# Optimization experiments

Hardware: AMD Instinct MI355X
Metric: run time of the kernel (lower is better)

## Reference

```python
import jax, jax.numpy as jnp
import numpy as np

EPS = 1e-5
KS = 3  # deformable kernel size
K2 = KS * KS


def conv2d(x, w, stride=1, padding=1):
    return jax.lax.conv_general_dilated(
        x, w, window_strides=(stride, stride),
        padding=[(padding, padding), (padding, padding)],
        dimension_numbers=("NCHW", "OIHW", "NCHW"))


def batchnorm(x, gamma, beta):
    # training-mode BN: batch statistics over (N, H, W)
    mean = jnp.mean(x, axis=(0, 2, 3), keepdims=True)
    var = jnp.var(x, axis=(0, 2, 3), keepdims=True)
    xhat = (x - mean) * jax.lax.rsqrt(var + EPS)
    return xhat * gamma[None, :, None, None] + beta[None, :, None, None]


def deform_conv(x, offsets, w, pad=1):
    # x: (B,C,H,W); offsets: (B,2*K2,H,W) -> first K2 channels = row (y)
    # offsets, next K2 = col (x) offsets; w: (O,C,KS,KS)
    B, C, H, W = x.shape
    xp = jnp.pad(x, ((0, 0), (0, 0), (pad, pad), (pad, pad)))
    Hp, Wp = H + 2 * pad, W + 2 * pad
    # base grid (center of each output pixel in padded coords)
    p0_y = jnp.arange(H, dtype=x.dtype) + pad            # (H,)
    p0_x = jnp.arange(W, dtype=x.dtype) + pad            # (W,)
    # kernel tap offsets in [-1, 0, 1]^2, row-major
    pn = jnp.stack(jnp.meshgrid(jnp.arange(KS) - pad, jnp.arange(KS) - pad,
                                indexing="ij"), axis=-1).reshape(K2, 2).astype(x.dtype)
    off = offsets.reshape(B, 2, K2, H, W)
    off_y = jnp.transpose(off[:, 0], (0, 2, 3, 1))       # (B,H,W,K2)
    off_x = jnp.transpose(off[:, 1], (0, 2, 3, 1))
    py = p0_y[None, :, None, None] + pn[:, 0][None, None, None, :] + off_y
    px = p0_x[None, None, :, None] + pn[:, 1][None, None, None, :] + off_x
    py = jnp.clip(py, 0.0, Hp - 1.0)
    px = jnp.clip(px, 0.0, Wp - 1.0)
    y0 = jnp.floor(py).astype(jnp.int32)
    x0 = jnp.floor(px).astype(jnp.int32)
    y1 = jnp.minimum(y0 + 1, Hp - 1)
    x1 = jnp.minimum(x0 + 1, Wp - 1)
    wy = (py - y0.astype(x.dtype))[:, None]              # (B,1,H,W,K2)
    wx = (px - x0.astype(x.dtype))[:, None]

    def gather(xb, yi, xi):                              # xb (C,Hp,Wp)
        return xb[:, yi, xi]                             # (C,H,W,K2)
    g = jax.vmap(gather)
    v00 = g(xp, y0, x0)
    v01 = g(xp, y0, x1)
    v10 = g(xp, y1, x0)
    v11 = g(xp, y1, x1)
    sampled = (v00 * (1 - wy) * (1 - wx) + v01 * (1 - wy) * wx +
               v10 * wy * (1 - wx) + v11 * wy * wx)      # (B,C,H,W,K2)
    return jnp.einsum("bchwk,ock->bohw", sampled, w.reshape(w.shape[0], C, K2))


def setup_inputs() -> dict:
    key = jax.random.key(0)
    ks = jax.random.split(key, 16)
    B, Cin, P, H, W = 64, 64, 64, 64, 64
    s = lambda k, shp, fan: jax.random.normal(k, shp, jnp.float32) * (fan ** -0.5)
    return {
        "x": jax.random.normal(ks[0], (B, Cin, H, W), jnp.float32),
        "conv1_w": s(ks[1], (P, Cin, 3, 3), Cin * 9),
        "bn1_g": jnp.ones((P,), jnp.float32), "bn1_b": jnp.zeros((P,), jnp.float32),
        "conv2_w": s(ks[2], (16, P, 1, 1), P),
        "bn2_g": jnp.ones((16,), jnp.float32), "bn2_b": jnp.zeros((16,), jnp.float32),
        "off_w": s(ks[3], (18, 16, 3, 3), 16 * 9) * 0.1,
        "off_b": jnp.zeros((18,), jnp.float32),
        "conv3_w": s(ks[4], (16, 16, 3, 3), 16 * 9),
        "bn3_g": jnp.ones((16,), jnp.float32), "bn3_b": jnp.zeros((16,), jnp.float32),
        "conv4_w": s(ks[5], (P, 16, 3, 3), 16 * 9),
        "bn4_g": jnp.ones((P,), jnp.float32), "bn4_b": jnp.zeros((P,), jnp.float32),
    }


def reference(x, conv1_w, bn1_g, bn1_b, conv2_w, bn2_g, bn2_b, off_w, off_b,
              conv3_w, bn3_g, bn3_b, conv4_w, bn4_g, bn4_b):
    out = jax.nn.relu(batchnorm(conv2d(x, conv1_w, 1, 1), bn1_g, bn1_b))
    out = jax.nn.relu(batchnorm(conv2d(out, conv2_w, 1, 0), bn2_g, bn2_b))
    offsets = conv2d(out, off_w, 1, 1) + off_b[None, :, None, None]
    out = jax.nn.relu(batchnorm(deform_conv(out, offsets, conv3_w), bn3_g, bn3_b))
    out = batchnorm(conv2d(out, conv4_w, 1, 1), bn4_g, bn4_b)
    out = out + x  # identity shortcut (stride=1, in_planes==planes)
    return jax.nn.relu(out)
```

## Files before the change

kernel.cpp:

```cpp
#include <hip/hip_runtime.h>

#define BN_N 262144.0f

typedef unsigned short u16;
typedef __attribute__((ext_vector_type(8))) short short8;
typedef __attribute__((ext_vector_type(4))) float floatx4;

static __device__ __forceinline__ u16 f2bf(float f) {
  union { float f; unsigned u; } v; v.f = f;
  unsigned u = v.u;
  return (u16)((u + 0x7FFFu + ((u >> 16) & 1u)) >> 16);
}
static __device__ __forceinline__ float bf2f(u16 h) {
  union { unsigned u; float f; } v; v.u = ((unsigned)h) << 16;
  return v.f;
}

__global__ __launch_bounds__(256) void prep_w_k(const float* __restrict__ w1,
                                                u16* __restrict__ Bsw) {
  int d = blockIdx.x * 256 + threadIdx.x;
  int kin = d & 7, n = (d >> 3) & 63, kgrp = (d >> 9) & 3, kc = d >> 11;
  int k = kc * 32 + kgrp * 8 + kin;
  int tap = k >> 6, c = k & 63;
  Bsw[d] = f2bf(w1[n * 576 + c * 9 + tap]);
}

__global__ __launch_bounds__(256) void prep_w4_k(const float* __restrict__ w4,
                                                 u16* __restrict__ Bsw4) {
  int d = blockIdx.x * 256 + threadIdx.x;
  if (d >= 10240) return;
  int kin = d & 7, n = (d >> 3) & 63, lk = (d >> 9) & 3, kk = d >> 11;
  int tap = kk * 2 + (lk >> 1);
  int c = ((lk & 1) << 3) + kin;
  float v = (tap < 9) ? w4[n * 144 + c * 9 + tap] : 0.f;
  Bsw4[d] = f2bf(v);
}

__global__ __launch_bounds__(256) void prep_w3_k(const float* __restrict__ w3,
                                                 u16* __restrict__ Bsw3) {
  int d = blockIdx.x * 256 + threadIdx.x;
  if (d >= 2560) return;
  int kin = d & 7, n = (d >> 3) & 15, lk = (d >> 7) & 3, kk = d >> 9;
  int k = kk * 32 + lk * 8 + kin;
  int tap = k >> 4, c = k & 15;
  float v = (tap < 9) ? w3[n * 144 + c * 9 + tap] : 0.f;
  Bsw3[d] = f2bf(v);
}

__global__ __launch_bounds__(256) void prep_wo_k(const float* __restrict__ ow,
                                                 u16* __restrict__ BswO) {
  int d = blockIdx.x * 256 + threadIdx.x;
  if (d >= 5120) return;
  int kin = d & 7, n = (d >> 3) & 31, lk = (d >> 8) & 3, kk = d >> 10;
  int tap = kk * 2 + (lk >> 1);
  int c = ((lk & 1) << 3) + kin;
  float v = (tap < 9 && n < 18) ? ow[n * 144 + c * 9 + tap] : 0.f;
  BswO[d] = f2bf(v);
}

__global__ __launch_bounds__(256) void prep_x_k(const float* __restrict__ x,
                                                u16* __restrict__ xp) {
  int yp = blockIdx.x;
  int b = blockIdx.y;
  int tid = threadIdx.x;
  u16* rowbase = xp + ((size_t)(b * 66 + yp)) * 66 * 64;
  if (yp == 0 || yp == 65) {
    for (int i = tid; i < 1056; i += 256)
      ((ushort4*)rowbase)[i] = make_ushort4(0, 0, 0, 0);
    return;
  }
  int y = yp - 1;
  __shared__ u16 s[64][68];
  for (int i = tid; i < 4096; i += 256) {
    int c = i >> 6, xx = i & 63;
    s[xx][c] = f2bf(x[((b * 64 + c) << 12) + (y << 6) + xx]);
  }
  if (tid < 128) {
    int c = tid & 63;
    int xpad = (tid >> 6) ? 65 : 0;
    rowbase[xpad * 64 + c] = 0;
  }
  __syncthreads();
  for (int j = tid; j < 1024; j += 256) {
    int xx = j >> 4, c4 = (j & 15) << 2;
    *(ushort4*)(rowbase + (xx + 1) * 64 + c4) =
        make_ushort4(s[xx][c4], s[xx][c4 + 1], s[xx][c4 + 2], s[xx][c4 + 3]);
  }
}

__global__ __launch_bounds__(256) void conv1_mfma(const u16* __restrict__ xp,
                                                  const u16* __restrict__ Bsw,
                                                  u16* __restrict__ h1,
                                                  float* __restrict__ sum1, float* __restrict__ sq1) {
  const int tid = threadIdx.x;
  const int w = tid >> 6, l = tid & 63;
  const int lm = l & 15, lk = l >> 4;
  const int b = blockIdx.x >> 4;
  const int y = ((blockIdx.x & 15) << 2) + w;
  const u16* xpb = xp + (size_t)b * 66 * 66 * 64;

  floatx4 acc[4][4];
#pragma unroll
  for (int mt = 0; mt < 4; ++mt)
#pragma unroll
    for (int nb = 0; nb < 4; ++nb)
      acc[mt][nb] = (floatx4){0.f, 0.f, 0.f, 0.f};

  short8 aC[4], bC[4], aN[4], bN[4];

#define C1_LOAD(KK, A, BV)                                              \
  {                                                                     \
    const int tap_ = (KK) >> 1;                                         \
    const int dy_ = tap_ / 3, dx_ = tap_ - dy_ * 3;                     \
    const int c0_ = (((KK) & 1) << 5) + (lk << 3);                      \
    const u16* rowp_ = xpb + (((y + dy_) * 66) + lm + dx_) * 64 + c0_;  \
    A[0] = *(const short8*)(rowp_);                                     \
    A[1] = *(const short8*)(rowp_ + 16 * 64);                           \
    A[2] = *(const short8*)(rowp_ + 32 * 64);                           \
    A[3] = *(const short8*)(rowp_ + 48 * 64);                           \
    const u16* bp_ = Bsw + ((((KK) * 4 + lk) * 64) + lm) * 8;           \
    BV[0] = *(const short8*)(bp_);                                      \
    BV[1] = *(const short8*)(bp_ + 128);                                \
    BV[2] = *(const short8*)(bp_ + 256);                                \
    BV[3] = *(const short8*)(bp_ + 384);                                \
  }

  C1_LOAD(0, aC, bC)
#pragma unroll
  for (int kk = 0; kk < 18; ++kk) {
    if (kk < 17) C1_LOAD(kk + 1, aN, bN)
#pragma unroll
    for (int mt = 0; mt < 4; ++mt)
#pragma unroll
      for (int nb = 0; nb < 4; ++nb)
        acc[mt][nb] = __builtin_amdgcn_mfma_f32_16x16x32_bf16(aC[mt], bC[nb], acc[mt][nb], 0, 0, 0);
#pragma unroll
    for (int i = 0; i < 4; ++i) { aC[i] = aN[i]; bC[i] = bN[i]; }
  }
#undef C1_LOAD

#pragma unroll
  for (int mt = 0; mt < 4; ++mt)
#pragma unroll
    for (int nb = 0; nb < 4; ++nb) {
      u16* dst = h1 + ((size_t)(b * 64 + nb * 16 + lm) << 12) + (y << 6) + mt * 16 + (lk << 2);
      floatx4 v = acc[mt][nb];
      *(ushort4*)dst = make_ushort4(f2bf(v.x), f2bf(v.y), f2bf(v.z), f2bf(v.w));
    }

  __shared__ float lsum[4][64], lsq[4][64];
  float s[4], s2[4];
#pragma unroll
  for (int nb = 0; nb < 4; ++nb) {
    s[nb] = 0.f; s2[nb] = 0.f;
#pragma unroll
    for (int mt = 0; mt < 4; ++mt) {
      floatx4 a = acc[mt][nb];
      s[nb] += a.x + a.y + a.z + a.w;
      s2[nb] += a.x * a.x + a.y * a.y + a.z * a.z + a.w * a.w;
    }
    s[nb] += __shfl_xor(s[nb], 16, 64);  s[nb] += __shfl_xor(s[nb], 32, 64);
    s2[nb] += __shfl_xor(s2[nb], 16, 64); s2[nb] += __shfl_xor(s2[nb], 32, 64);
  }
  if (lk == 0) {
#pragma unroll
    for (int nb = 0; nb < 4; ++nb) { lsum[w][nb * 16 + lm] = s[nb]; lsq[w][nb * 16 + lm] = s2[nb]; }
  }
  __syncthreads();
  if (tid < 64) atomicAdd(&sum1[tid], lsum[0][tid] + lsum[1][tid] + lsum[2][tid] + lsum[3][tid]);
  else if (tid < 128) { int o = tid - 64; atomicAdd(&sq1[o], lsq[0][o] + lsq[1][o] + lsq[2][o] + lsq[3][o]); }
}

__global__ __launch_bounds__(256) void conv2_k(const u16* __restrict__ h1,
                                               const float* __restrict__ w2,
                                               const float* __restrict__ sum1, const float* __restrict__ sq1,
                                               const float* __restrict__ g1, const float* __restrict__ b1,
                                               float* __restrict__ out,
                                               float* __restrict__ sum2, float* __restrict__ sq2) {
  __shared__ float s_wt[64 * 16];
  __shared__ float s_scale[64], s_shift[64];
  __shared__ float ls[4][16], lsq[4][16];
  int tid = threadIdx.x;
  for (int i = tid; i < 1024; i += 256) {
    int o = i >> 6, c = i & 63;
    s_wt[c * 16 + o] = w2[i];
  }
  if (tid < 64) {
    float m = sum1[tid] / BN_N;
    float var = sq1[tid] / BN_N - m * m;
    float sc = g1[tid] * rsqrtf(var + 1e-5f);
    s_scale[tid] = sc;
    s_shift[tid] = b1[tid] - m * sc;
  }
  __syncthreads();
  int p = blockIdx.x * 256 + tid;
  int b = p >> 12, r = p & 4095;
  const u16* src = h1 + ((size_t)b << 18) + r;
  float acc[16];
#pragma unroll
  for (int o = 0; o < 16; ++o) acc[o] = 0.f;
  for (int c = 0; c < 64; ++c) {
    float v = bf2f(src[c << 12]);
    v = fmaxf(v * s_scale[c] + s_shift[c], 0.f);
    const float* wp = &s_wt[c * 16];
    float4 w0 = *(const float4*)wp;
    float4 w1 = *(const float4*)(wp + 4);
    float4 w2v = *(const float4*)(wp + 8);
    float4 w3v = *(const float4*)(wp + 12);
    acc[0] += w0.x * v;  acc[1] += w0.y * v;  acc[2] += w0.z * v;  acc[3] += w0.w * v;
    acc[4] += w1.x * v;  acc[5] += w1.y * v;  acc[6] += w1.z * v;  acc[7] += w1.w * v;
    acc[8] += w2v.x * v; acc[9] += w2v.y * v; acc[10] += w2v.z * v; acc[11] += w2v.w * v;
    acc[12] += w3v.x * v; acc[13] += w3v.y * v; acc[14] += w3v.z * v; acc[15] += w3v.w * v;
  }
  float* dst = out + (size_t)p * 16;
#pragma unroll
  for (int c4 = 0; c4 < 4; ++c4)
    *(float4*)(dst + c4 * 4) = make_float4(acc[c4*4], acc[c4*4+1], acc[c4*4+2], acc[c4*4+3]);
  int lane = tid & 63, wv = tid >> 6;
#pragma unroll
  for (int o = 0; o < 16; ++o) {
    float s = acc[o], s2 = acc[o] * acc[o];
#pragma unroll
    for (int off = 32; off > 0; off >>= 1) {
      s += __shfl_down(s, off, 64);
      s2 += __shfl_down(s2, off, 64);
    }
    if (lane == 0) { ls[wv][o] = s; lsq[wv][o] = s2; }
  }
  __syncthreads();
  if (tid < 16) atomicAdd(&sum2[tid], ls[0][tid] + ls[1][tid] + ls[2][tid] + ls[3][tid]);
  else if (tid < 32) {
    int o = tid - 16;
    atomicAdd(&sq2[o], lsq[0][o] + lsq[1][o] + lsq[2][o] + lsq[3][o]);
  }
}

__global__ __launch_bounds__(256) void bnrelu2_k(const float* __restrict__ ws2,
                                                 const float* __restrict__ sum2, const float* __restrict__ sq2,
                                                 const float* __restrict__ g2, const float* __restrict__ b2,
                                                 u16* __restrict__ h2p) {
  __shared__ float s_scale[16], s_shift[16];
  int tid = threadIdx.x;
  if (tid < 16) {
    float m = sum2[tid] / BN_N;
    float var = sq2[tid] / BN_N - m * m;
    float sc = g2[tid] * rsqrtf(var + 1e-5f);
    s_scale[tid] = sc;
    s_shift[tid] = b2[tid] - m * sc;
  }
  __syncthreads();
  int p = blockIdx.x * 256 + tid;
  int b = p >> 12, r = p & 4095;
  int y = r >> 6, xx = r & 63;
  const float* src = ws2 + (size_t)p * 16;
  u16* dst = h2p + (size_t)(((b * 66) + y + 1) * 66 + xx + 1) * 16;
#pragma unroll
  for (int c4 = 0; c4 < 4; ++c4) {
    float4 v = *(const float4*)(src + c4 * 4);
    u16 o0 = f2bf(fmaxf(v.x * s_scale[c4*4]   + s_shift[c4*4],   0.f));
    u16 o1 = f2bf(fmaxf(v.y * s_scale[c4*4+1] + s_shift[c4*4+1], 0.f));
    u16 o2 = f2bf(fmaxf(v.z * s_scale[c4*4+2] + s_shift[c4*4+2], 0.f));
    u16 o3 = f2bf(fmaxf(v.w * s_scale[c4*4+3] + s_shift[c4*4+3], 0.f));
    *(ushort4*)(dst + c4 * 4) = make_ushort4(o0, o1, o2, o3);
  }
}

__global__ __launch_bounds__(256) void offconv_mfma(const u16* __restrict__ h2p,
                                                    const u16* __restrict__ BswO,
                                                    const float* __restrict__ ob,
                                                    float* __restrict__ offs) {
  const int tid = threadIdx.x;
  const int w = tid >> 6, l = tid & 63;
  const int lm = l & 15, lk = l >> 4;
  const int b = blockIdx.x >> 4;
  const int y = ((blockIdx.x & 15) << 2) + w;
  const u16* hb = h2p + (size_t)b * 66 * 66 * 16;

  floatx4 acc[4][2];
#pragma unroll
  for (int mt = 0; mt < 4; ++mt)
#pragma unroll
    for (int nb = 0; nb < 2; ++nb)
      acc[mt][nb] = (floatx4){0.f, 0.f, 0.f, 0.f};

  short8 aC[4], bC[2], aN[4], bN[2];

#define OC_LOAD(KK, A, BV)                                                    \
  {                                                                           \
    int tap_ = (KK) * 2 + (lk >> 1);                                          \
    if (tap_ > 8) tap_ = 8;                                                   \
    const int dy_ = tap_ / 3, dx_ = tap_ - dy_ * 3;                           \
    const int c0_ = (lk & 1) << 3;                                            \
    const u16* rowp_ = hb + (size_t)(((y + dy_) * 66) + lm + dx_) * 16 + c0_; \
    A[0] = *(const short8*)(rowp_);                                           \
    A[1] = *(const short8*)(rowp_ + 16 * 16);                                 \
    A[2] = *(const short8*)(rowp_ + 32 * 16);                                 \
    A[3] = *(const short8*)(rowp_ + 48 * 16);                                 \
    const u16* bp_ = BswO + ((((KK) * 4 + lk) * 32) + lm) * 8;                \
    BV[0] = *(const short8*)(bp_);                                            \
    BV[1] = *(const short8*)(bp_ + 128);                                      \
  }

  OC_LOAD(0, aC, bC)
#pragma unroll
  for (int kk = 0; kk < 5; ++kk) {
    if (kk < 4) OC_LOAD(kk + 1, aN, bN)
#pragma unroll
    for (int mt = 0; mt < 4; ++mt)
#pragma unroll
      for (int nb = 0; nb < 2; ++nb)
        acc[mt][nb] = __builtin_amdgcn_mfma_f32_16x16x32_bf16(aC[mt], bC[nb], acc[mt][nb], 0, 0, 0);
#pragma unroll
    for (int i = 0; i < 4; ++i) aC[i] = aN[i];
    bC[0] = bN[0]; bC[1] = bN[1];
  }
#undef OC_LOAD

#pragma unroll
  for (int mt = 0; mt < 4; ++mt)
#pragma unroll
    for (int nb = 0; nb < 2; ++nb) {
      int oc = nb * 16 + lm;
      if (oc < 18) {
        float bias = ob[oc];
        floatx4 v = acc[mt][nb];
        v.x += bias; v.y += bias; v.z += bias; v.w += bias;
        float* dst = offs + (size_t)b * 73728 + (oc << 12) + (y << 6) + mt * 16 + (lk << 2);
        *(floatx4*)dst = v;
      }
    }
}

__global__ __launch_bounds__(256) void deform_mfma(const u16* __restrict__ h2p,
                                                   const float* __restrict__ offs,
                                                   const u16* __restrict__ Bsw3,
                                                   float* __restrict__ out,
                                                   float* __restrict__ sum3, float* __restrict__ sq3) {
  const int tid = threadIdx.x;
  const int w = tid >> 6, l = tid & 63;
  const int lm = l & 15, lk = l >> 4;
  const int pbase = blockIdx.x * 256 + w * 64;
  const int b = pbase >> 12;
  const u16* img = h2p + (size_t)b * 66 * 66 * 16;
  const float* offp = offs + (size_t)b * 73728;

  short8 bf[5];
#pragma unroll
  for (int kk = 0; kk < 5; ++kk)
    bf[kk] = *(const short8*)(Bsw3 + (((kk * 4 + lk) * 16) + lm) * 8);

  floatx4 acc[4];
#pragma unroll
  for (int mt = 0; mt < 4; ++mt) acc[mt] = (floatx4){0.f, 0.f, 0.f, 0.f};

#pragma unroll
  for (int mt = 0; mt < 4; ++mt) {
    const int p = pbase + mt * 16 + lm;
    const int r = p & 4095;
    const int y = r >> 6, x = r & 63;
#pragma unroll
    for (int kk = 0; kk < 5; ++kk) {
      const int k0 = kk * 32 + lk * 8;
      int tap = k0 >> 4;
      const int c0 = k0 & 15;
      if (tap > 8) tap = 8;
      const int dy = tap / 3, dx = tap - dy * 3;
      float offy = offp[(tap << 12) + r];
      float offx = offp[((tap + 9) << 12) + r];
      float py = (float)(y + dy) + offy;
      float px = (float)(x + dx) + offx;
      py = fminf(fmaxf(py, 0.f), 65.f);
      px = fminf(fmaxf(px, 0.f), 65.f);
      float y0f = floorf(py), x0f = floorf(px);
      int y0 = (int)y0f, x0 = (int)x0f;
      int y1 = min(y0 + 1, 65), x1 = min(x0 + 1, 65);
      float wy = py - y0f, wx = px - x0f;
      float w00 = (1.f - wy) * (1.f - wx), w01 = (1.f - wy) * wx;
      float w10 = wy * (1.f - wx),         w11 = wy * wx;
      short8 v00 = *(const short8*)(img + (y0 * 66 + x0) * 16 + c0);
      short8 v01 = *(const short8*)(img + (y0 * 66 + x1) * 16 + c0);
      short8 v10 = *(const short8*)(img + (y1 * 66 + x0) * 16 + c0);
      short8 v11 = *(const short8*)(img + (y1 * 66 + x1) * 16 + c0);
      short8 a;
#pragma unroll
      for (int j = 0; j < 8; ++j) {
        float s = bf2f((u16)v00[j]) * w00 + bf2f((u16)v01[j]) * w01
                + bf2f((u16)v10[j]) * w10 + bf2f((u16)v11[j]) * w11;
        a[j] = (short)f2bf(s);
      }
      acc[mt] = __builtin_amdgcn_mfma_f32_16x16x32_bf16(a, bf[kk], acc[mt], 0, 0, 0);
    }
  }

  float s = 0.f, s2 = 0.f;
#pragma unroll
  for (int mt = 0; mt < 4; ++mt) {
    floatx4 a = acc[mt];
    s += a.x + a.y + a.z + a.w;
    s2 += a.x * a.x + a.y * a.y + a.z * a.z + a.w * a.w;
#pragma unroll
    for (int reg = 0; reg < 4; ++reg) {
      int pp = pbase + mt * 16 + lk * 4 + reg;
      out[(size_t)pp * 16 + lm] = acc[mt][reg];
    }
  }
  __shared__ float ls[4][16], lsq[4][16];
  s += __shfl_xor(s, 16, 64);  s += __shfl_xor(s, 32, 64);
  s2 += __shfl_xor(s2, 16, 64); s2 += __shfl_xor(s2, 32, 64);
  if (lk == 0) { ls[w][lm] = s; lsq[w][lm] = s2; }
  __syncthreads();
  if (tid < 16) atomicAdd(&sum3[tid], ls[0][tid] + ls[1][tid] + ls[2][tid] + ls[3][tid]);
  else if (tid < 32) {
    int o = tid - 16;
    atomicAdd(&sq3[o], lsq[0][o] + lsq[1][o] + lsq[2][o] + lsq[3][o]);
  }
}

__global__ __launch_bounds__(256) void bnrelu3_k(const float* __restrict__ wsd,
                                                 const float* __restrict__ sum3, const float* __restrict__ sq3,
                                                 const float* __restrict__ g3, const float* __restrict__ b3,
                                                 u16* __restrict__ h3p) {
  __shared__ float s_scale[16], s_shift[16];
  int tid = threadIdx.x;
  if (tid < 16) {
    float m = sum3[tid] / BN_N;
    float var = sq3[tid] / BN_N - m * m;
    float sc = g3[tid] * rsqrtf(var + 1e-5f);
    s_scale[tid] = sc;
    s_shift[tid] = b3[tid] - m * sc;
  }
  __syncthreads();
  int p = blockIdx.x * 256 + tid;
  int b = p >> 12, r = p & 4095;
  int y = r >> 6, xx = r & 63;
  const float* src = wsd + (size_t)p * 16;
  u16* dst = h3p + (size_t)(((b * 66) + y + 1) * 66 + xx + 1) * 16;
#pragma unroll
  for (int c4 = 0; c4 < 4; ++c4) {
    float4 v = *(const float4*)(src + c4 * 4);
    u16 o0 = f2bf(fmaxf(v.x * s_scale[c4*4]   + s_shift[c4*4],   0.f));
    u16 o1 = f2bf(fmaxf(v.y * s_scale[c4*4+1] + s_shift[c4*4+1], 0.f));
    u16 o2 = f2bf(fmaxf(v.z * s_scale[c4*4+2] + s_shift[c4*4+2], 0.f));
    u16 o3 = f2bf(fmaxf(v.w * s_scale[c4*4+3] + s_shift[c4*4+3], 0.f));
    *(ushort4*)(dst + c4 * 4) = make_ushort4(o0, o1, o2, o3);
  }
}

__global__ __launch_bounds__(256) void conv4_mfma(const u16* __restrict__ h3p,
                                                  const u16* __restrict__ Bsw4,
                                                  u16* __restrict__ h4,
                                                  float* __restrict__ sum4, float* __restrict__ sq4) {
  const int tid = threadIdx.x;
  const int w = tid >> 6, l = tid & 63;
  const int lm = l & 15, lk = l >> 4;
  const int b = blockIdx.x >> 4;
  const int y = ((blockIdx.x & 15) << 2) + w;
  const u16* hb = h3p + (size_t)b * 66 * 66 * 16;

  floatx4 acc[4][4];
#pragma unroll
  for (int mt = 0; mt < 4; ++mt)
#pragma unroll
    for (int nb = 0; nb < 4; ++nb)
      acc[mt][nb] = (floatx4){0.f, 0.f, 0.f, 0.f};

  short8 aC[4], bC[4], aN[4], bN[4];

#define C4_LOAD(KK, A, BV)                                                    \
  {                                                                           \
    int tap_ = (KK) * 2 + (lk >> 1);                                          \
    if (tap_ > 8) tap_ = 8;                                                   \
    const int dy_ = tap_ / 3, dx_ = tap_ - dy_ * 3;                           \
    const int c0_ = (lk & 1) << 3;                                            \
    const u16* rowp_ = hb + (size_t)(((y + dy_) * 66) + lm + dx_) * 16 + c0_; \
    A[0] = *(const short8*)(rowp_);                                           \
    A[1] = *(const short8*)(rowp_ + 16 * 16);                                 \
    A[2] = *(const short8*)(rowp_ + 32 * 16);                                 \
    A[3] = *(const short8*)(rowp_ + 48 * 16);                                 \
    const u16* bp_ = Bsw4 + ((((KK) * 4 + lk) * 64) + lm) * 8;                \
    BV[0] = *(const short8*)(bp_);                                            \
    BV[1] = *(const short8*)(bp_ + 128);                                      \
    BV[2] = *(const short8*)(bp_ + 256);                                      \
    BV[3] = *(const short8*)(bp_ + 384);                                      \
  }

  C4_LOAD(0, aC, bC)
#pragma unroll
  for (int kk = 0; kk < 5; ++kk) {
    if (kk < 4) C4_LOAD(kk + 1, aN, bN)
#pragma unroll
    for (int mt = 0; mt < 4; ++mt)
#pragma unroll
      for (int nb = 0; nb < 4; ++nb)
        acc[mt][nb] = __builtin_amdgcn_mfma_f32_16x16x32_bf16(aC[mt], bC[nb], acc[mt][nb], 0, 0, 0);
#pragma unroll
    for (int i = 0; i < 4; ++i) { aC[i] = aN[i]; bC[i] = bN[i]; }
  }
#undef C4_LOAD

#pragma unroll
  for (int mt = 0; mt < 4; ++mt)
#pragma unroll
    for (int nb = 0; nb < 4; ++nb) {
      u16* dst = h4 + ((size_t)(b * 64 + nb * 16 + lm) << 12) + (y << 6) + mt * 16 + (lk << 2);
      floatx4 v = acc[mt][nb];
      *(ushort4*)dst = make_ushort4(f2bf(v.x), f2bf(v.y), f2bf(v.z), f2bf(v.w));
    }

  __shared__ float lsum[4][64], lsq[4][64];
  float s[4], s2[4];
#pragma unroll
  for (int nb = 0; nb < 4; ++nb) {
    s[nb] = 0.f; s2[nb] = 0.f;
#pragma unroll
    for (int mt = 0; mt < 4; ++mt) {
      floatx4 a = acc[mt][nb];
      s[nb] += a.x + a.y + a.z + a.w;
      s2[nb] += a.x * a.x + a.y * a.y + a.z * a.z + a.w * a.w;
    }
    s[nb] += __shfl_xor(s[nb], 16, 64);  s[nb] += __shfl_xor(s[nb], 32, 64);
    s2[nb] += __shfl_xor(s2[nb], 16, 64); s2[nb] += __shfl_xor(s2[nb], 32, 64);
  }
  if (lk == 0) {
#pragma unroll
    for (int nb = 0; nb < 4; ++nb) { lsum[w][nb * 16 + lm] = s[nb]; lsq[w][nb * 16 + lm] = s2[nb]; }
  }
  __syncthreads();
  if (tid < 64) atomicAdd(&sum4[tid], lsum[0][tid] + lsum[1][tid] + lsum[2][tid] + lsum[3][tid]);
  else if (tid < 128) { int o = tid - 64; atomicAdd(&sq4[o], lsq[0][o] + lsq[1][o] + lsq[2][o] + lsq[3][o]); }
}

__global__ __launch_bounds__(256) void final_k(const u16* __restrict__ h4,
                                               float* __restrict__ out,
                                               const float* __restrict__ x,
                                               const float* __restrict__ sum4, const float* __restrict__ sq4,
                                               const float* __restrict__ g4, const float* __restrict__ b4) {
  __shared__ float s_scale[64], s_shift[64];
  int tid = threadIdx.x;
  if (tid < 64) {
    float m = sum4[tid] / BN_N;
    float var = sq4[tid] / BN_N - m * m;
    float sc = g4[tid] * rsqrtf(var + 1e-5f);
    s_scale[tid] = sc;
    s_shift[tid] = b4[tid] - m * sc;
  }
  __syncthreads();
  int i = (blockIdx.x * 256 + tid) * 4;
  int c = (i >> 12) & 63;
  ushort4 q = *(const ushort4*)(h4 + i);
  float4 xv = *(const float4*)(x + i);
  float sc = s_scale[c], sh = s_shift[c];
  float4 v;
  v.x = fmaxf(bf2f(q.x) * sc + sh + xv.x, 0.f);
  v.y = fmaxf(bf2f(q.y) * sc + sh + xv.y, 0.f);
  v.z = fmaxf(bf2f(q.z) * sc + sh + xv.z, 0.f);
  v.w = fmaxf(bf2f(q.w) * sc + sh + xv.w, 0.f);
  *(float4*)(out + i) = v;
}

extern "C" void kernel_launch(void* const* d_in, const int* in_sizes, int n_in,
                              void* d_out, int out_size, void* d_ws, size_t ws_size,
                              hipStream_t stream) {
  const float* x  = (const float*)d_in[0];
  const float* w1 = (const float*)d_in[1];
  const float* g1 = (const float*)d_in[2];
  const float* b1 = (const float*)d_in[3];
  const float* w2 = (const float*)d_in[4];
  const float* g2 = (const float*)d_in[5];
  const float* b2 = (const float*)d_in[6];
  const float* ow = (const float*)d_in[7];
  const float* ob = (const float*)d_in[8];
  const float* w3 = (const float*)d_in[9];
  const float* g3 = (const float*)d_in[10];
  const float* b3 = (const float*)d_in[11];
  const float* w4 = (const float*)d_in[12];
  const float* g4 = (const float*)d_in[13];
  const float* b4 = (const float*)d_in[14];
  float* out = (float*)d_out;
  float* ws = (float*)d_ws;

  float* offs = ws;
  float* wsd  = offs + 4718592;
  float* ws2  = wsd + 4194304;
  float* h2pf = ws2 + 4194304;
  float* stats = h2pf + 4460544;
  float* sum1 = stats, *sq1 = stats + 64;
  float* sum2 = stats + 128, *sq2 = stats + 144;
  float* sum3 = stats + 160, *sq3 = stats + 176;
  float* sum4 = stats + 192, *sq4 = stats + 256;
  u16* xp   = (u16*)ws;
  u16* Bsw  = (u16*)(stats + 320);
  u16* Bsw4 = Bsw + 36864;
  u16* Bsw3 = Bsw4 + 10240;
  u16* BswO = Bsw3 + 2560;
  u16* h2p  = (u16*)h2pf;
  u16* h4   = (u16*)offs;
  u16* h1   = (u16*)out;

  hipMemsetAsync(stats, 0, 320 * sizeof(float), stream);
  hipMemsetAsync(h2p, 0, 4460544 * sizeof(u16), stream);

  prep_w_k<<<144, 256, 0, stream>>>(w1, Bsw);
  prep_w4_k<<<40, 256, 0, stream>>>(w4, Bsw4);
  prep_w3_k<<<10, 256, 0, stream>>>(w3, Bsw3);
  prep_wo_k<<<20, 256, 0, stream>>>(ow, BswO);
  prep_x_k<<<dim3(66, 64), 256, 0, stream>>>(x, xp);
  conv1_mfma<<<1024, 256, 0, stream>>>(xp, Bsw, h1, sum1, sq1);
  conv2_k<<<1024, 256, 0, stream>>>(h1, w2, sum1, sq1, g1, b1, ws2, sum2, sq2);
  bnrelu2_k<<<1024, 256, 0, stream>>>(ws2, sum2, sq2, g2, b2, h2p);
  offconv_mfma<<<1024, 256, 0, stream>>>(h2p, BswO, ob, offs);
  deform_mfma<<<1024, 256, 0, stream>>>(h2p, offs, Bsw3, wsd, sum3, sq3);
  bnrelu3_k<<<1024, 256, 0, stream>>>(wsd, sum3, sq3, g3, b3, h2p );
  conv4_mfma<<<1024, 256, 0, stream>>>(h2p, Bsw4, h4, sum4, sq4);
  final_k<<<16384, 256, 0, stream>>>(h4, out, x, sum4, sq4, g4, b4);
}
```

Baseline: 361.5 us.

## Stage conv input rows in LDS via global_load_lds with swizzled/padded layouts

The conv1, offset-conv and conv4 kernels now copy their input row band (and, for the small convs, their weights) into shared memory with direct global-to-LDS loads, then read MFMA operands from LDS instead of issuing repeated global loads per tap. The padded input layouts change to support this: the 64-channel buffer uses an XOR chunk swizzle and the 16-channel buffer pads each pixel to 24 elements to reduce bank conflicts. The deform and bnrelu kernels are updated to the new stride. This adds large LDS allocations that may limit occupancy and drops the software register prefetch of A operands. It also grows the memset of the padded buffer.

```diff
diff --git a/kernel.cpp b/kernel.cpp
--- a/kernel.cpp
+++ b/kernel.cpp
@@ -5,6 +5,12 @@
 typedef unsigned short u16;
 typedef __attribute__((ext_vector_type(8))) short short8;
 typedef __attribute__((ext_vector_type(4))) float floatx4;
+
+#define RP1 4224
+#define IS1 278784
+#define RP2 1584
+#define IS2 104544
+#define H2P_TOTAL 6690816
 
 static __device__ __forceinline__ u16 f2bf(float f) {
   union { float f; unsigned u; } v; v.f = f;
@@ -14,6 +20,10 @@
 static __device__ __forceinline__ float bf2f(u16 h) {
   union { unsigned u; float f; } v; v.u = ((unsigned)h) << 16;
   return v.f;
+}
+static __device__ __forceinline__ void cp16(const u16* g, u16* l) {
+  __builtin_amdgcn_global_load_lds((const __attribute__((address_space(1))) unsigned int*)g,
+                                   (__attribute__((address_space(3))) unsigned int*)l, 16, 0, 0);
 }
 
 __global__ __launch_bounds__(256) void prep_w_k(const float* __restrict__ w1,
@@ -63,28 +73,29 @@
   int yp = blockIdx.x;
   int b = blockIdx.y;
   int tid = threadIdx.x;
-  u16* rowbase = xp + ((size_t)(b * 66 + yp)) * 66 * 64;
+  u16* rowbase = xp + (size_t)(b * 66 + yp) * RP1;
   if (yp == 0 || yp == 65) {
-    for (int i = tid; i < 1056; i += 256)
+    for (int i = tid; i < RP1 / 4; i += 256)
       ((ushort4*)rowbase)[i] = make_ushort4(0, 0, 0, 0);
     return;
   }
   int y = yp - 1;
-  __shared__ u16 s[64][68];
+  __shared__ __align__(16) u16 s[64][72];
   for (int i = tid; i < 4096; i += 256) {
     int c = i >> 6, xx = i & 63;
     s[xx][c] = f2bf(x[((b * 64 + c) << 12) + (y << 6) + xx]);
   }
   if (tid < 128) {
     int c = tid & 63;
-    int xpad = (tid >> 6) ? 65 : 0;
-    rowbase[xpad * 64 + c] = 0;
-  }
-  __syncthreads();
-  for (int j = tid; j < 1024; j += 256) {
-    int xx = j >> 4, c4 = (j & 15) << 2;
-    *(ushort4*)(rowbase + (xx + 1) * 64 + c4) =
-        make_ushort4(s[xx][c4], s[xx][c4 + 1], s[xx][c4 + 2], s[xx][c4 + 3]);
+    int pxp = (tid >> 6) ? 65 : 0;
+    rowbase[pxp * 64 + c] = 0;
+  }
+  __syncthreads();
+  for (int j = tid; j < 512; j += 256) {
+    int xx = j >> 3, chunk = j & 7;
+    int pxp = xx + 1;
+    int ph = chunk ^ (pxp & 7);
+    *(short8*)(rowbase + pxp * 64 + ph * 8) = *(const short8*)(&s[xx][chunk * 8]);
   }
 }
 
@@ -92,12 +103,17 @@
                                                   const u16* __restrict__ Bsw,
                                                   u16* __restrict__ h1,
                                                   float* __restrict__ sum1, float* __restrict__ sq1) {
+  __shared__ __align__(16) u16 lA[25600];
   const int tid = threadIdx.x;
   const int w = tid >> 6, l = tid & 63;
   const int lm = l & 15, lk = l >> 4;
   const int b = blockIdx.x >> 4;
-  const int y = ((blockIdx.x & 15) << 2) + w;
-  const u16* xpb = xp + (size_t)b * 66 * 66 * 64;
+  const int y0 = (blockIdx.x & 15) << 2;
+  const int y = y0 + w;
+  const u16* src = xp + ((size_t)b * 66 + y0) * RP1;
+  for (int seg = w; seg < 50; seg += 4)
+    cp16(src + seg * 512 + l * 8, lA + seg * 512);
+  __syncthreads();
 
   floatx4 acc[4][4];
 #pragma unroll
@@ -106,38 +122,39 @@
     for (int nb = 0; nb < 4; ++nb)
       acc[mt][nb] = (floatx4){0.f, 0.f, 0.f, 0.f};
 
-  short8 aC[4], bC[4], aN[4], bN[4];
-
-#define C1_LOAD(KK, A, BV)                                              \
-  {                                                                     \
-    const int tap_ = (KK) >> 1;                                         \
-    const int dy_ = tap_ / 3, dx_ = tap_ - dy_ * 3;                     \
-    const int c0_ = (((KK) & 1) << 5) + (lk << 3);                      \
-    const u16* rowp_ = xpb + (((y + dy_) * 66) + lm + dx_) * 64 + c0_;  \
-    A[0] = *(const short8*)(rowp_);                                     \
-    A[1] = *(const short8*)(rowp_ + 16 * 64);                           \
-    A[2] = *(const short8*)(rowp_ + 32 * 64);                           \
-    A[3] = *(const short8*)(rowp_ + 48 * 64);                           \
-    const u16* bp_ = Bsw + ((((KK) * 4 + lk) * 64) + lm) * 8;           \
-    BV[0] = *(const short8*)(bp_);                                      \
-    BV[1] = *(const short8*)(bp_ + 128);                                \
-    BV[2] = *(const short8*)(bp_ + 256);                                \
-    BV[3] = *(const short8*)(bp_ + 384);                                \
-  }
-
-  C1_LOAD(0, aC, bC)
+  short8 bC[4], bN[4];
+#define BLOAD(KK, BV)                                                 \
+  { const u16* bp_ = Bsw + ((((KK) * 4 + lk) * 64) + lm) * 8;         \
+    BV[0] = *(const short8*)(bp_);                                    \
+    BV[1] = *(const short8*)(bp_ + 128);                              \
+    BV[2] = *(const short8*)(bp_ + 256);                              \
+    BV[3] = *(const short8*)(bp_ + 384); }
+
+  BLOAD(0, bC)
 #pragma unroll
   for (int kk = 0; kk < 18; ++kk) {
-    if (kk < 17) C1_LOAD(kk + 1, aN, bN)
+    if (kk < 17) BLOAD(kk + 1, bN)
+    const int tap = kk >> 1;
+    const int dy = (tap < 3) ? 0 : ((tap < 6) ? 1 : 2);
+    const int dx = tap - dy * 3;
+    const int chunk = ((kk & 1) << 2) + lk;
+    const int rowoff = (w + dy) * RP1;
+    short8 aF[4];
+#pragma unroll
+    for (int mt = 0; mt < 4; ++mt) {
+      int pxp = mt * 16 + lm + dx;
+      int ph = chunk ^ (pxp & 7);
+      aF[mt] = *(const short8*)(lA + rowoff + pxp * 64 + ph * 8);
+    }
 #pragma unroll
     for (int mt = 0; mt < 4; ++mt)
 #pragma unroll
       for (int nb = 0; nb < 4; ++nb)
-        acc[mt][nb] = __builtin_amdgcn_mfma_f32_16x16x32_bf16(aC[mt], bC[nb], acc[mt][nb], 0, 0, 0);
-#pragma unroll
-    for (int i = 0; i < 4; ++i) { aC[i] = aN[i]; bC[i] = bN[i]; }
-  }
-#undef C1_LOAD
+        acc[mt][nb] = __builtin_amdgcn_mfma_f32_16x16x32_bf16(aF[mt], bC[nb], acc[mt][nb], 0, 0, 0);
+#pragma unroll
+    for (int i = 0; i < 4; ++i) bC[i] = bN[i];
+  }
+#undef BLOAD
 
 #pragma unroll
   for (int mt = 0; mt < 4; ++mt)
@@ -148,7 +165,9 @@
       *(ushort4*)dst = make_ushort4(f2bf(v.x), f2bf(v.y), f2bf(v.z), f2bf(v.w));
     }
 
-  __shared__ float lsum[4][64], lsq[4][64];
+  __syncthreads();
+  float* LS = (float*)lA;
+  float* LQ = LS + 256;
   float s[4], s2[4];
 #pragma unroll
   for (int nb = 0; nb < 4; ++nb) {
@@ -164,11 +183,11 @@
   }
   if (lk == 0) {
 #pragma unroll
-    for (int nb = 0; nb < 4; ++nb) { lsum[w][nb * 16 + lm] = s[nb]; lsq[w][nb * 16 + lm] = s2[nb]; }
-  }
-  __syncthreads();
-  if (tid < 64) atomicAdd(&sum1[tid], lsum[0][tid] + lsum[1][tid] + lsum[2][tid] + lsum[3][tid]);
-  else if (tid < 128) { int o = tid - 64; atomicAdd(&sq1[o], lsq[0][o] + lsq[1][o] + lsq[2][o] + lsq[3][o]); }
+    for (int nb = 0; nb < 4; ++nb) { LS[w * 64 + nb * 16 + lm] = s[nb]; LQ[w * 64 + nb * 16 + lm] = s2[nb]; }
+  }
+  __syncthreads();
+  if (tid < 64) atomicAdd(&sum1[tid], LS[tid] + LS[64 + tid] + LS[128 + tid] + LS[192 + tid]);
+  else if (tid < 128) { int o = tid - 64; atomicAdd(&sq1[o], LQ[o] + LQ[64 + o] + LQ[128 + o] + LQ[192 + o]); }
 }
 
 __global__ __launch_bounds__(256) void conv2_k(const u16* __restrict__ h1,
@@ -253,7 +272,7 @@
   int b = p >> 12, r = p & 4095;
   int y = r >> 6, xx = r & 63;
   const float* src = ws2 + (size_t)p * 16;
-  u16* dst = h2p + (size_t)(((b * 66) + y + 1) * 66 + xx + 1) * 16;
+  u16* dst = h2p + (size_t)(b * 66 + y + 1) * RP2 + (xx + 1) * 24;
 #pragma unroll
   for (int c4 = 0; c4 < 4; ++c4) {
     float4 v = *(const float4*)(src + c4 * 4);
@@ -269,12 +288,18 @@
                                                     const u16* __restrict__ BswO,
                                                     const float* __restrict__ ob,
                                                     float* __restrict__ offs) {
+  __shared__ __align__(16) u16 lA[9728];
+  __shared__ __align__(16) u16 lB[5120];
   const int tid = threadIdx.x;
   const int w = tid >> 6, l = tid & 63;
   const int lm = l & 15, lk = l >> 4;
   const int b = blockIdx.x >> 4;
-  const int y = ((blockIdx.x & 15) << 2) + w;
-  const u16* hb = h2p + (size_t)b * 66 * 66 * 16;
+  const int y0 = (blockIdx.x & 15) << 2;
+  const int y = y0 + w;
+  const u16* src = h2p + ((size_t)b * 66 + y0) * RP2;
+  for (int seg = w; seg < 19; seg += 4) cp16(src + seg * 512 + l * 8, lA + seg * 512);
+  for (int seg = w; seg < 10; seg += 4) cp16(BswO + seg * 512 + l * 8, lB + seg * 512);
+  __syncthreads();
 
   floatx4 acc[4][2];
 #pragma unroll
@@ -283,38 +308,26 @@
     for (int nb = 0; nb < 2; ++nb)
       acc[mt][nb] = (floatx4){0.f, 0.f, 0.f, 0.f};
 
-  short8 aC[4], bC[2], aN[4], bN[2];
-
-#define OC_LOAD(KK, A, BV)                                                    \
-  {                                                                           \
-    int tap_ = (KK) * 2 + (lk >> 1);                                          \
-    if (tap_ > 8) tap_ = 8;                                                   \
-    const int dy_ = tap_ / 3, dx_ = tap_ - dy_ * 3;                           \
-    const int c0_ = (lk & 1) << 3;                                            \
-    const u16* rowp_ = hb + (size_t)(((y + dy_) * 66) + lm + dx_) * 16 + c0_; \
-    A[0] = *(const short8*)(rowp_);                                           \
-    A[1] = *(const short8*)(rowp_ + 16 * 16);                                 \
-    A[2] = *(const short8*)(rowp_ + 32 * 16);                                 \
-    A[3] = *(const short8*)(rowp_ + 48 * 16);                                 \
-    const u16* bp_ = BswO + ((((KK) * 4 + lk) * 32) + lm) * 8;                \
-    BV[0] = *(const short8*)(bp_);                                            \
-    BV[1] = *(const short8*)(bp_ + 128);                                      \
-  }
-
-  OC_LOAD(0, aC, bC)
 #pragma unroll
   for (int kk = 0; kk < 5; ++kk) {
-    if (kk < 4) OC_LOAD(kk + 1, aN, bN)
+    int tap = kk * 2 + (lk >> 1);
+    if (tap > 8) tap = 8;
+    const int dy = tap / 3, dx = tap - dy * 3;
+    const int c0 = (lk & 1) << 3;
+    const int rowoff = (w + dy) * RP2;
+    short8 aF[4], bF[2];
 #pragma unroll
     for (int mt = 0; mt < 4; ++mt)
+      aF[mt] = *(const short8*)(lA + rowoff + (mt * 16 + lm + dx) * 24 + c0);
+    const u16* bp = lB + (((kk * 4 + lk) * 32) + lm) * 8;
+    bF[0] = *(const short8*)(bp);
+    bF[1] = *(const short8*)(bp + 128);
+#pragma unroll
+    for (int mt = 0; mt < 4; ++mt)
 #pragma unroll
       for (int nb = 0; nb < 2; ++nb)
-        acc[mt][nb] = __builtin_amdgcn_mfma_f32_16x16x32_bf16(aC[mt], bC[nb], acc[mt][nb], 0, 0, 0);
-#pragma unroll
-    for (int i = 0; i < 4; ++i) aC[i] = aN[i];
-    bC[0] = bN[0]; bC[1] = bN[1];
-  }
-#undef OC_LOAD
+        acc[mt][nb] = __builtin_amdgcn_mfma_f32_16x16x32_bf16(aF[mt], bF[nb], acc[mt][nb], 0, 0, 0);
+  }
 
 #pragma unroll
   for (int mt = 0; mt < 4; ++mt)
@@ -341,7 +354,7 @@
   const int lm = l & 15, lk = l >> 4;
   const int pbase = blockIdx.x * 256 + w * 64;
   const int b = pbase >> 12;
-  const u16* img = h2p + (size_t)b * 66 * 66 * 16;
+  const u16* img = h2p + (size_t)b * IS2;
   const float* offp = offs + (size_t)b * 73728;
 
   short8 bf[5];
@@ -377,10 +390,10 @@
       float wy = py - y0f, wx = px - x0f;
       float w00 = (1.f - wy) * (1.f - wx), w01 = (1.f - wy) * wx;
       float w10 = wy * (1.f - wx),         w11 = wy * wx;
-      short8 v00 = *(const short8*)(img + (y0 * 66 + x0) * 16 + c0);
-      short8 v01 = *(const short8*)(img + (y0 * 66 + x1) * 16 + c0);
-      short8 v10 = *(const short8*)(img + (y1 * 66 + x0) * 16 + c0);
-      short8 v11 = *(const short8*)(img + (y1 * 66 + x1) * 16 + c0);
+      short8 v00 = *(const short8*)(img + (y0 * 66 + x0) * 24 + c0);
+      short8 v01 = *(const short8*)(img + (y0 * 66 + x1) * 24 + c0);
+      short8 v10 = *(const short8*)(img + (y1 * 66 + x0) * 24 + c0);
+      short8 v11 = *(const short8*)(img + (y1 * 66 + x1) * 24 + c0);
       short8 a;
 #pragma unroll
       for (int j = 0; j < 8; ++j) {
@@ -434,7 +447,7 @@
   int b = p >> 12, r = p & 4095;
   int y = r >> 6, xx = r & 63;
   const float* src = wsd + (size_t)p * 16;
-  u16* dst = h3p + (size_t)(((b * 66) + y + 1) * 66 + xx + 1) * 16;
+  u16* dst = h3p + (size_t)(b * 66 + y + 1) * RP2 + (xx + 1) * 24;
 #pragma unroll
   for (int c4 = 0; c4 < 4; ++c4) {
     float4 v = *(const float4*)(src + c4 * 4);
@@ -450,12 +463,18 @@
                                                   const u16* __restrict__ Bsw4,
                                                   u16* __restrict__ h4,
                                                   float* __restrict__ sum4, float* __restrict__ sq4) {
+  __shared__ __align__(16) u16 lA[9728];
+  __shared__ __align__(16) u16 lB[10240];
   const int tid = threadIdx.x;
   const int w = tid >> 6, l = tid & 63;
   const int lm = l & 15, lk = l >> 4;
   const int b = blockIdx.x >> 4;
-  const int y = ((blockIdx.x & 15) << 2) + w;
-  const u16* hb = h3p + (size_t)b * 66 * 66 * 16;
+  const int y0 = (blockIdx.x & 15) << 2;
+  const int y = y0 + w;
+  const u16* src = h3p + ((size_t)b * 66 + y0) * RP2;
+  for (int seg = w; seg < 19; seg += 4) cp16(src + seg * 512 + l * 8, lA + seg * 512);
+  for (int seg = w; seg < 20; seg += 4) cp16(Bsw4 + seg * 512 + l * 8, lB + seg * 512);
+  __syncthreads();
 
   floatx4 acc[4][4];
 #pragma unroll
@@ -464,39 +483,28 @@
     for (int nb = 0; nb < 4; ++nb)
       acc[mt][nb] = (floatx4){0.f, 0.f, 0.f, 0.f};
 
-  short8 aC[4], bC[4], aN[4], bN[4];
-
-#define C4_LOAD(KK, A, BV)                                                    \
-  {                                                                           \
-    int tap_ = (KK) * 2 + (lk >> 1);                                          \
-    if (tap_ > 8) tap_ = 8;                                                   \
-    const int dy_ = tap_ / 3, dx_ = tap_ - dy_ * 3;                           \
-    const int c0_ = (lk & 1) << 3;                                            \
-    const u16* rowp_ = hb + (size_t)(((y + dy_) * 66) + lm + dx_) * 16 + c0_; \
-    A[0] = *(const short8*)(rowp_);                                           \
-    A[1] = *(const short8*)(rowp_ + 16 * 16);                                 \
-    A[2] = *(const short8*)(rowp_ + 32 * 16);                                 \
-    A[3] = *(const short8*)(rowp_ + 48 * 16);                                 \
-    const u16* bp_ = Bsw4 + ((((KK) * 4 + lk) * 64) + lm) * 8;                \
-    BV[0] = *(const short8*)(bp_);                                            \
-    BV[1] = *(const short8*)(bp_ + 128);                                      \
-    BV[2] = *(const short8*)(bp_ + 256);                                      \
-    BV[3] = *(const short8*)(bp_ + 384);                                      \
-  }
-
-  C4_LOAD(0, aC, bC)
 #pragma unroll
   for (int kk = 0; kk < 5; ++kk) {
-    if (kk < 4) C4_LOAD(kk + 1, aN, bN)
+    int tap = kk * 2 + (lk >> 1);
+    if (tap > 8) tap = 8;
+    const int dy = tap / 3, dx = tap - dy * 3;
+    const int c0 = (lk & 1) << 3;
+    const int rowoff = (w + dy) * RP2;
+    short8 aF[4], bF[4];
 #pragma unroll
     for (int mt = 0; mt < 4; ++mt)
+      aF[mt] = *(const short8*)(lA + rowoff + (mt * 16 + lm + dx) * 24 + c0);
+    const u16* bp = lB + (((kk * 4 + lk) * 64) + lm) * 8;
+    bF[0] = *(const short8*)(bp);
+    bF[1] = *(const short8*)(bp + 128);
+    bF[2] = *(const short8*)(bp + 256);
+    bF[3] = *(const short8*)(bp + 384);
+#pragma unroll
+    for (int mt = 0; mt < 4; ++mt)
 #pragma unroll
       for (int nb = 0; nb < 4; ++nb)
-        acc[mt][nb] = __builtin_amdgcn_mfma_f32_16x16x32_bf16(aC[mt], bC[nb], acc[mt][nb], 0, 0, 0);
-#pragma unroll
-    for (int i = 0; i < 4; ++i) { aC[i] = aN[i]; bC[i] = bN[i]; }
-  }
-#undef C4_LOAD
+        acc[mt][nb] = __builtin_amdgcn_mfma_f32_16x16x32_bf16(aF[mt], bF[nb], acc[mt][nb], 0, 0, 0);
+  }
 
 #pragma unroll
   for (int mt = 0; mt < 4; ++mt)
@@ -507,7 +515,9 @@
       *(ushort4*)dst = make_ushort4(f2bf(v.x), f2bf(v.y), f2bf(v.z), f2bf(v.w));
     }
 
-  __shared__ float lsum[4][64], lsq[4][64];
+  __syncthreads();
+  float* LS = (float*)lA;
+  float* LQ = LS + 256;
   float s[4], s2[4];
 #pragma unroll
   for (int nb = 0; nb < 4; ++nb) {
@@ -523,11 +533,11 @@
   }
   if (lk == 0) {
 #pragma unroll
-    for (int nb = 0; nb < 4; ++nb) { lsum[w][nb * 16 + lm] = s[nb]; lsq[w][nb * 16 + lm] = s2[nb]; }
-  }
-  __syncthreads();
-  if (tid < 64) atomicAdd(&sum4[tid], lsum[0][tid] + lsum[1][tid] + lsum[2][tid] + lsum[3][tid]);
-  else if (tid < 128) { int o = tid - 64; atomicAdd(&sq4[o], lsq[0][o] + lsq[1][o] + lsq[2][o] + lsq[3][o]); }
+    for (int nb = 0; nb < 4; ++nb) { LS[w * 64 + nb * 16 + lm] = s[nb]; LQ[w * 64 + nb * 16 + lm] = s2[nb]; }
+  }
+  __syncthreads();
+  if (tid < 64) atomicAdd(&sum4[tid], LS[tid] + LS[64 + tid] + LS[128 + tid] + LS[192 + tid]);
+  else if (tid < 128) { int o = tid - 64; atomicAdd(&sq4[o], LQ[o] + LQ[64 + o] + LQ[128 + o] + LQ[192 + o]); }
 }
 
 __global__ __launch_bounds__(256) void final_k(const u16* __restrict__ h4,
@@ -598,7 +608,7 @@
   u16* h1   = (u16*)out;
 
   hipMemsetAsync(stats, 0, 320 * sizeof(float), stream);
-  hipMemsetAsync(h2p, 0, 4460544 * sizeof(u16), stream);
+  hipMemsetAsync(h2p, 0, (size_t)H2P_TOTAL * sizeof(u16), stream);
 
   prep_w_k<<<144, 256, 0, stream>>>(w1, Bsw);
   prep_w4_k<<<40, 256, 0, stream>>>(w4, Bsw4);
```

Result: faster. 334.9 us (-7.4%).
